# Kernel optimization log

Measured on AMD Instinct MI355X. Metric: run time of the kernel, lower is better.

## Reference

```python
import jax, jax.numpy as jnp
import numpy as np
import math

DIM = 4096
HAD_SCALE = 1.0 / math.sqrt(DIM)  # orthonormal Hadamard normalization


def fwht(x):
    """Fast Walsh-Hadamard transform over the last axis.

    x: (B, N) with N a power of two. log2(N) butterfly stages,
    each stage vectorized over the whole batch.
    """
    B, N = x.shape
    h = 1
    while h < N:
        # view as (B, N/(2h), 2, h): pairs at stride h
        x = x.reshape(B, N // (2 * h), 2, h)
        a = x[:, :, 0, :]
        b = x[:, :, 1, :]
        x = jnp.stack([a + b, a - b], axis=2).reshape(B, N)
        h *= 2
    return x


def setup_inputs() -> dict:
    key = jax.random.key(0)
    x = jax.random.normal(key, (16384, DIM), dtype=jnp.float32)
    return {"x": x}


def reference(x) -> jnp.ndarray:
    # Hadamard.forward: transform_fn(x.contiguous(), had_scale)
    return fwht(x) * jnp.asarray(HAD_SCALE, dtype=x.dtype)
```

## Files before the change

### kernel.cpp

```cpp
#include <hip/hip_runtime.h>

constexpr int DIM = 4096;

__device__ __forceinline__ float4 f4add(float4 a, float4 b) {
    return make_float4(a.x + b.x, a.y + b.y, a.z + b.z, a.w + b.w);
}
__device__ __forceinline__ float4 f4sub(float4 a, float4 b) {
    return make_float4(a.x - b.x, a.y - b.y, a.z - b.z, a.w - b.w);
}

__device__ __forceinline__ float4 fwht4_inner(float4 v) {
    float a = v.x + v.y, b = v.x - v.y;
    float c = v.z + v.w, d = v.z - v.w;
    return make_float4(a + c, b + d, a - c, b - d);
}

__device__ __forceinline__ void fwht16(float* v) {
#pragma unroll
    for (int s = 1; s < 16; s <<= 1) {
#pragma unroll
        for (int m = 0; m < 16; ++m) {
            if (!(m & s)) {
                float a = v[m], b = v[m ^ s];
                v[m]     = a + b;
                v[m ^ s] = a - b;
            }
        }
    }
}


__global__ __launch_bounds__(256, 4) void fwht_kernel(const float* __restrict__ x,
                                                      float* __restrict__ out) {
    __shared__ float lds0[DIM];
    __shared__ float lds1[DIM];

    const int t = threadIdx.x;
    const size_t base = (size_t)blockIdx.x * DIM;

    const float4* X4 = reinterpret_cast<const float4*>(x + base);
    float4 f0 = X4[t];
    float4 f1 = X4[256 + t];
    float4 f2 = X4[512 + t];
    float4 f3 = X4[768 + t];

    f0 = fwht4_inner(f0);
    f1 = fwht4_inner(f1);
    f2 = fwht4_inner(f2);
    f3 = fwht4_inner(f3);
    {
        float4 s0 = f4add(f0, f1), d0 = f4sub(f0, f1);
        float4 s1 = f4add(f2, f3), d1 = f4sub(f2, f3);
        f0 = f4add(s0, s1);
        f1 = f4add(d0, d1);
        f2 = f4sub(s0, s1);
        f3 = f4sub(d0, d1);
    }

    {
        const int dbase = (t << 2) ^ (((t >> 4) & 3) << 4);
        float4* L = reinterpret_cast<float4*>(lds0);
        L[(((0 << 10) | dbase) ^ (0 << 2)) >> 2] = f0;
        L[(((1 << 10) | dbase) ^ (1 << 2)) >> 2] = f1;
        L[(((2 << 10) | dbase) ^ (2 << 2)) >> 2] = f2;
        L[(((3 << 10) | dbase) ^ (3 << 2)) >> 2] = f3;
    }
    __syncthreads();

    float w[16];
    {
        const int c  = t & 3;
        const int j  = (t >> 2) & 3;
        const int th = t >> 4;
        const int b  = (j << 10) | (th << 6) | c;
        const int xo = (j << 2) ^ ((th & 3) << 4);
#pragma unroll
        for (int m = 0; m < 16; ++m)
            w[m] = lds0[b | ((m << 2) ^ xo)];
    }

    fwht16(w);

    {
        const int c  = t & 3;
        const int j  = (t >> 2) & 3;
        const int th = t >> 4;
        const int b  = (j << 10) | (th << 6) | c;
        const int xo = (j << 2) ^ ((th & 3) << 4);
#pragma unroll
        for (int m = 0; m < 16; ++m)
            lds1[b | ((m << 2) ^ xo)] = w[m];
    }
    __syncthreads();

    float z[16];
    const int c2 = t & 3;
    const int tl = (t >> 2) & 15;
    const int j2 = t >> 6;
    {
        const int b2 = (j2 << 10) | (tl << 2) | c2;
        const int xb = b2 ^ (j2 << 2);
#pragma unroll
        for (int n = 0; n < 16; ++n)
            z[n] = lds1[(xb ^ ((n & 3) << 4)) | (n << 6)];
    }

    fwht16(z);

    float* O = out + base;
    const int ob = (j2 << 10) | (tl << 2) | c2;
#pragma unroll
    for (int n = 0; n < 16; ++n)
        O[ob | (n << 6)] = z[n] * 0.015625f;
}

extern "C" void kernel_launch(void* const* d_in, const int* in_sizes, int n_in,
                              void* d_out, int out_size, void* d_ws, size_t ws_size,
                              hipStream_t stream) {
    const float* x = (const float*)d_in[0];
    float* out = (float*)d_out;
    const int rows = in_sizes[0] / DIM;
    fwht_kernel<<<rows, 256, 0, stream>>>(x, out);
}
```

Baseline: 96.40 us.

## Make first LDS exchange wave-local, drop a barrier, use nontemporal loads/stores

```diff
diff --git a/kernel.cpp b/kernel.cpp
--- a/kernel.cpp
+++ b/kernel.cpp
@@ -1,18 +1,14 @@
 #include <hip/hip_runtime.h>
 
 constexpr int DIM = 4096;
+using f32x4 = __attribute__((ext_vector_type(4))) float;
 
-__device__ __forceinline__ float4 f4add(float4 a, float4 b) {
-    return make_float4(a.x + b.x, a.y + b.y, a.z + b.z, a.w + b.w);
-}
-__device__ __forceinline__ float4 f4sub(float4 a, float4 b) {
-    return make_float4(a.x - b.x, a.y - b.y, a.z - b.z, a.w - b.w);
-}
-
-__device__ __forceinline__ float4 fwht4_inner(float4 v) {
+__device__ __forceinline__ f32x4 fwht4_inner(f32x4 v) {
     float a = v.x + v.y, b = v.x - v.y;
     float c = v.z + v.w, d = v.z - v.w;
-    return make_float4(a + c, b + d, a - c, b - d);
+    f32x4 r;
+    r.x = a + c; r.y = b + d; r.z = a - c; r.w = b - d;
+    return r;
 }
 
 __device__ __forceinline__ void fwht16(float* v) {
@@ -32,86 +28,80 @@
 
 __global__ __launch_bounds__(256, 4) void fwht_kernel(const float* __restrict__ x,
                                                       float* __restrict__ out) {
-    __shared__ float lds0[DIM];
+    __shared__ f32x4 lds0v[DIM / 4];
     __shared__ float lds1[DIM];
+    float* lds0 = reinterpret_cast<float*>(lds0v);
 
     const int t = threadIdx.x;
+    const int l = t & 63;
+    const int w = t >> 6;
     const size_t base = (size_t)blockIdx.x * DIM;
 
-    const float4* X4 = reinterpret_cast<const float4*>(x + base);
-    float4 f0 = X4[t];
-    float4 f1 = X4[256 + t];
-    float4 f2 = X4[512 + t];
-    float4 f3 = X4[768 + t];
+    const f32x4* X4 = reinterpret_cast<const f32x4*>(x + base);
+    f32x4 f0 = __builtin_nontemporal_load(X4 + t);
+    f32x4 f1 = __builtin_nontemporal_load(X4 + 256 + t);
+    f32x4 f2 = __builtin_nontemporal_load(X4 + 512 + t);
+    f32x4 f3 = __builtin_nontemporal_load(X4 + 768 + t);
 
     f0 = fwht4_inner(f0);
     f1 = fwht4_inner(f1);
     f2 = fwht4_inner(f2);
     f3 = fwht4_inner(f3);
     {
-        float4 s0 = f4add(f0, f1), d0 = f4sub(f0, f1);
-        float4 s1 = f4add(f2, f3), d1 = f4sub(f2, f3);
-        f0 = f4add(s0, s1);
-        f1 = f4add(d0, d1);
-        f2 = f4sub(s0, s1);
-        f3 = f4sub(d0, d1);
+        f32x4 s0 = f0 + f1, d0 = f0 - f1;
+        f32x4 s1 = f2 + f3, d1 = f2 - f3;
+        f0 = s0 + s1;
+        f1 = d0 + d1;
+        f2 = s0 - s1;
+        f3 = d0 - d1;
     }
 
     {
-        const int dbase = (t << 2) ^ (((t >> 4) & 3) << 4);
-        float4* L = reinterpret_cast<float4*>(lds0);
-        L[(((0 << 10) | dbase) ^ (0 << 2)) >> 2] = f0;
-        L[(((1 << 10) | dbase) ^ (1 << 2)) >> 2] = f1;
-        L[(((2 << 10) | dbase) ^ (2 << 2)) >> 2] = f2;
-        L[(((3 << 10) | dbase) ^ (3 << 2)) >> 2] = f3;
+        f32x4* R = lds0v + (w << 8);
+        const int b0 = (l << 2) ^ (((l >> 4) & 3) << 2);
+        R[b0 >> 2]                  = f0;
+        R[((b0 ^ 16) | 256) >> 2]   = f1;
+        R[(b0 | 512) >> 2]          = f2;
+        R[((b0 ^ 16) | 768) >> 2]   = f3;
     }
-    __syncthreads();
+    asm volatile("s_waitcnt lgkmcnt(0)" ::: "memory");
 
-    float w[16];
+    float wv[16];
+    const int c1 = l & 3;
+    const int h1 = (l >> 2) & 3;
+    const int j1 = l >> 4;
     {
-        const int c  = t & 3;
-        const int j  = (t >> 2) & 3;
-        const int th = t >> 4;
-        const int b  = (j << 10) | (th << 6) | c;
-        const int xo = (j << 2) ^ ((th & 3) << 4);
+        float* Rf = lds0 + (w << 10);
+        const int rb = (c1 | (h1 << 6) | (j1 << 8)) ^ (h1 << 2) ^ ((j1 & 1) << 4);
 #pragma unroll
         for (int m = 0; m < 16; ++m)
-            w[m] = lds0[b | ((m << 2) ^ xo)];
+            wv[m] = Rf[rb ^ (m << 2)];
     }
 
-    fwht16(w);
+    fwht16(wv);
 
     {
-        const int c  = t & 3;
-        const int j  = (t >> 2) & 3;
-        const int th = t >> 4;
-        const int b  = (j << 10) | (th << 6) | c;
-        const int xo = (j << 2) ^ ((th & 3) << 4);
+        const int tb = (c1 | (h1 << 6) | (w << 8) | (j1 << 10)) ^ (h1 << 2) ^ ((j1 & 1) << 4);
 #pragma unroll
         for (int m = 0; m < 16; ++m)
-            lds1[b | ((m << 2) ^ xo)] = w[m];
+            lds1[tb ^ (m << 2)] = wv[m];
     }
     __syncthreads();
 
     float z[16];
-    const int c2 = t & 3;
-    const int tl = (t >> 2) & 15;
-    const int j2 = t >> 6;
     {
-        const int b2 = (j2 << 10) | (tl << 2) | c2;
-        const int xb = b2 ^ (j2 << 2);
+        const int qb = (l | (w << 10)) ^ ((w & 1) << 4);
 #pragma unroll
         for (int n = 0; n < 16; ++n)
-            z[n] = lds1[(xb ^ ((n & 3) << 4)) | (n << 6)];
+            z[n] = lds1[qb ^ (n << 6) ^ ((n & 3) << 2)];
     }
 
     fwht16(z);
 
-    float* O = out + base;
-    const int ob = (j2 << 10) | (tl << 2) | c2;
+    float* O = out + base + (w << 10) + l;
 #pragma unroll
     for (int n = 0; n < 16; ++n)
-        O[ob | (n << 6)] = z[n] * 0.015625f;
+        __builtin_nontemporal_store(z[n] * 0.015625f, O + (n << 6));
 }
 
 extern "C" void kernel_launch(void* const* d_in, const int* in_sizes, int n_in,
```

New measurement: 85.96 us. 1.12x faster.
